# Performance work log

Measured on AMD Instinct MI355X. Metric: run time of the kernel, lower is better.

## Reference

```python
import jax, jax.numpy as jnp
import numpy as np

BN = 1024      # B*N voxel groups
M = 32         # points per voxel
D_MODEL = 128
D_POINTS = 64


def _mlp(x, w1, b1, w2, b2):
    # Linear -> ReLU -> Linear (torch nn.Sequential equivalent)
    return jax.nn.relu(x @ w1 + b1) @ w2 + b2


def setup_inputs() -> dict:
    key = jax.random.key(0)
    ks = jax.random.split(key, 16)
    def lin(k, din, dout):
        return (jax.random.normal(k, (din, dout), jnp.float32) / np.sqrt(din)).astype(jnp.float32)
    inp = {}
    inp["pv_xyz"] = jax.random.normal(ks[0], (BN, M, 3), jnp.float32)
    inp["features"] = jax.random.normal(ks[1], (BN, M, D_POINTS), jnp.float32)
    i = 2
    for name, din in [("alpha", 3), ("beta", 3), ("delta", 3), ("epsilon", D_MODEL), ("omega", D_POINTS)]:
        inp[f"{name}_w1"] = lin(ks[i], din, D_MODEL); i += 1
        inp[f"{name}_b1"] = jnp.zeros((D_MODEL,), jnp.float32)
        inp[f"{name}_w2"] = lin(ks[i], D_MODEL, D_MODEL); i += 1
        inp[f"{name}_b2"] = jnp.zeros((D_MODEL,), jnp.float32)
    return inp


def reference(pv_xyz, features,
              alpha_w1, alpha_b1, alpha_w2, alpha_b2,
              beta_w1, beta_b1, beta_w2, beta_b2,
              delta_w1, delta_b1, delta_w2, delta_b2,
              epsilon_w1, epsilon_b1, epsilon_w2, epsilon_b2,
              omega_w1, omega_b1, omega_w2, omega_b2):
    # abs relative position: [BN, M, M, 3]
    dist = jnp.abs(pv_xyz[:, :, None, :] - pv_xyz[:, None, :, :])
    pij = _mlp(dist, delta_w1, delta_b1, delta_w2, delta_b2)          # [BN,M,M,D]
    q = _mlp(pv_xyz, alpha_w1, alpha_b1, alpha_w2, alpha_b2)          # [BN,M,D]
    k = _mlp(pv_xyz, beta_w1, beta_b1, beta_w2, beta_b2)              # [BN,M,D]
    v = _mlp(features, omega_w1, omega_b1, omega_w2, omega_b2)        # [BN,M,D]
    scale = jnp.float32(1.0 / np.sqrt(D_MODEL))
    w = _mlp((q[:, :, None, :] - k[:, None, :, :] + pij) * scale,
             epsilon_w1, epsilon_b1, epsilon_w2, epsilon_b2)          # [BN,M,M,D]
    wij = jax.nn.softmax(w, axis=-2)                                  # softmax over key axis
    # torch.einsum('bmmf,bmf->bmf', wij, v): repeated index -> diagonal of wij
    midx = jnp.arange(wij.shape[1])
    res = wij[:, midx, midx, :] * v                                   # [BN,M,D]
    return jnp.concatenate([res, features], axis=-1)                  # [BN,M,D+C]
```

## Files before the change

### kernel.cpp

```cpp
#include <hip/hip_runtime.h>
#include <hip/hip_bf16.h>
#include <cstdint>
#include <cstddef>


#define SCALE 0.08838834764831843f

typedef __bf16 bf16x8 __attribute__((ext_vector_type(8)));
typedef float f32x16 __attribute__((ext_vector_type(16)));

__device__ __forceinline__ ushort f2b(float f){
  __hip_bfloat16 h = __float2bfloat16(f);
  return __builtin_bit_cast(ushort, h);
}
__device__ __forceinline__ float b2f(uint32_t s){
  union { uint32_t u; float f; } x; x.u = s << 16; return x.f;
}
__device__ __forceinline__ uint32_t pk2(float a, float b){
  union { __hip_bfloat162 h2; uint32_t u; } x;
  x.h2.x = __float2bfloat16(a); x.h2.y = __float2bfloat16(b);
  return x.u;
}
__device__ __forceinline__ f32x16 MFMA(uint4 a, uint4 b, f32x16 c){
  return __builtin_amdgcn_mfma_f32_32x32x16_bf16(
      __builtin_bit_cast(bf16x8, a), __builtin_bit_cast(bf16x8, b), c, 0, 0, 0);
}

__global__ __launch_bounds__(256) void k_pre(
    const float* __restrict__ A2, const float* __restrict__ B2, const float* __restrict__ D2,
    const float* __restrict__ E1, const float* __restrict__ E2,
    const float* __restrict__ O1, const float* __restrict__ O2,
    const float* __restrict__ ab2, const float* __restrict__ bb2, const float* __restrict__ db2,
    const float* __restrict__ eb1,
    const float* __restrict__ D1, const float* __restrict__ db1,
    ushort* __restrict__ aep, ushort* __restrict__ bep, ushort* __restrict__ gtp,
    ushort* __restrict__ e2p, ushort* __restrict__ o2p, ushort* __restrict__ o1t,
    ushort* __restrict__ d1p, float* __restrict__ c0)
{
  const int bid = blockIdx.x, tid = threadIdx.x;
  if (bid < 192){
    const float* W = (bid < 64) ? A2 : (bid < 128) ? B2 : D2;
    ushort* dst    = (bid < 64) ? aep : (bid < 128) ? bep : gtp;
    int flat = (bid & 63)*256 + tid;
    int co = flat >> 10, rem = flat & 1023, h = rem >> 3, i = rem & 7;
    int r = co*8 + i;
    float acc = 0.f;
    for (int t = 0; t < 128; ++t) acc = fmaf(W[r*128 + t], E1[t*128 + h], acc);
    dst[(co*128 + h)*8 + i] = f2b(acc * SCALE);
  } else if (bid < 256){
    int flat = (bid - 192)*256 + tid;
    int co = flat >> 10, rem = flat & 1023, d = rem >> 3, i = rem & 7;
    e2p[(co*128 + d)*8 + i] = f2b(E2[(co*8 + i)*128 + d]);
  } else if (bid < 320){
    int flat = (bid - 256)*256 + tid;
    int co = flat >> 10, rem = flat & 1023, d = rem >> 3, i = rem & 7;
    o2p[(co*128 + d)*8 + i] = f2b(O2[(co*8 + i)*128 + d]);
  } else if (bid < 352){
    int flat = (bid - 320)*256 + tid;
    int fo = flat >> 10, rem = flat & 1023, o = rem >> 3, e = rem & 7;
    o1t[(fo*128 + o)*8 + e] = f2b(O1[(fo*8 + e)*128 + o]);
  } else if (bid < 360){
    int flat = (bid - 352)*256 + tid;
    int koct = flat >> 10, cd = (flat >> 3) & 127, e = flat & 7;
    float val = 0.f;
    if (koct == 0){
      if (e < 3) val = D1[e*128 + cd];
      else if (e == 3) val = db1[cd];
    }
    d1p[flat] = f2b(val);
  } else {
    if (tid < 128){
      float acc = 0.f;
      for (int t = 0; t < 128; ++t) acc = fmaf(ab2[t] - bb2[t] + db2[t], E1[t*128 + tid], acc);
      c0[tid] = acc * SCALE + eb1[tid];
    }
  }
}

__device__ __forceinline__ void gemm64x128(const ushort (*sa)[64][8], const ushort (*sw)[128][8],
                                           int w, int l31, int hl, int p0,
                                           const float* __restrict__ bias,
                                           ushort* __restrict__ dst)
{
  const int rw = w >> 1, ctb = (w & 1) * 2;
  f32x16 acc0, acc1;
#pragma unroll
  for (int r = 0; r < 16; ++r){ acc0[r] = 0.f; acc1[r] = 0.f; }
#pragma unroll
  for (int kk = 0; kk < 8; ++kk){
    uint4 a  = *(const uint4*)&sa[2*kk + hl][32*rw + l31][0];
    uint4 b0 = *(const uint4*)&sw[2*kk + hl][32*ctb + l31][0];
    uint4 b1 = *(const uint4*)&sw[2*kk + hl][32*(ctb+1) + l31][0];
    acc0 = MFMA(a, b0, acc0);
    acc1 = MFMA(a, b1, acc1);
  }
#pragma unroll
  for (int t = 0; t < 2; ++t){
    const f32x16 acc = t ? acc1 : acc0;
    const int d = 32*(ctb + t) + l31;
    const float bv = bias ? bias[d] : 0.f;
#pragma unroll
    for (int r = 0; r < 16; ++r){
      int row = 32*rw + (r & 3) + 8*(r >> 2) + 4*hl;
      dst[(size_t)(p0 + row)*128 + d] = f2b(acc[r] + bv);
    }
  }
}

__global__ __launch_bounds__(256, 2) void k_point(
    const float* __restrict__ pv, const float* __restrict__ feat,
    const float* __restrict__ A1, const float* __restrict__ ab1,
    const float* __restrict__ B1, const float* __restrict__ bb1,
    const float* __restrict__ ob1, const float* __restrict__ ob2,
    const float* __restrict__ c0,
    const uint4* __restrict__ aep, const uint4* __restrict__ bep,
    const uint4* __restrict__ o1t, const uint4* __restrict__ o2p,
    ushort* __restrict__ qe_ws, ushort* __restrict__ ke_ws, ushort* __restrict__ v_ws,
    float* __restrict__ out)
{
  __shared__ ushort sW[16][128][8];
  __shared__ ushort sA[16][64][8];
  __shared__ ushort sF[8][64][8];
  __shared__ float  sLw[3][128];
  __shared__ float  sLb[128];
  __shared__ float  sLb2[128];

  const int tid = threadIdx.x;
  const int p0  = blockIdx.x * 64;
  const int w = tid >> 6, lane = tid & 63, l31 = lane & 31, hl = lane >> 5;

  for (int idx = tid; idx < 64*16; idx += 256){
    int p = idx >> 4, k4 = idx & 15;
    float4 f = ((const float4*)(feat + (size_t)(p0 + p)*64))[k4];
    ((float4*)(out + (size_t)(p0 + p)*192 + 128))[k4] = f;
  }

  for (int idx = tid; idx < 2048; idx += 256) ((uint4*)sW)[idx] = aep[idx];
  for (int idx = tid; idx < 384; idx += 256) ((float*)sLw)[idx] = A1[idx];
  if (tid < 128) sLb[tid] = ab1[tid];
  __syncthreads();
  {
    int p = tid & 63, ob = tid >> 6;
    float x0 = pv[(size_t)(p0+p)*3+0], x1 = pv[(size_t)(p0+p)*3+1], x2 = pv[(size_t)(p0+p)*3+2];
#pragma unroll
    for (int it = 0; it < 4; ++it){
      int oct = ob + 4*it;
      float h[8];
#pragma unroll
      for (int e = 0; e < 8; ++e){
        int cd = oct*8 + e;
        float t = fmaf(x0, sLw[0][cd], fmaf(x1, sLw[1][cd], fmaf(x2, sLw[2][cd], sLb[cd])));
        h[e] = fmaxf(t, 0.f);
      }
      uint4 u; u.x = pk2(h[0],h[1]); u.y = pk2(h[2],h[3]); u.z = pk2(h[4],h[5]); u.w = pk2(h[6],h[7]);
      *(uint4*)&sA[oct][p][0] = u;
    }
  }
  __syncthreads();
  gemm64x128(sA, sW, w, l31, hl, p0, c0, qe_ws);
  __syncthreads();

  for (int idx = tid; idx < 2048; idx += 256) ((uint4*)sW)[idx] = bep[idx];
  for (int idx = tid; idx < 384; idx += 256) ((float*)sLw)[idx] = B1[idx];
  if (tid < 128) sLb[tid] = bb1[tid];
  __syncthreads();
  {
    int p = tid & 63, ob = tid >> 6;
    float x0 = pv[(size_t)(p0+p)*3+0], x1 = pv[(size_t)(p0+p)*3+1], x2 = pv[(size_t)(p0+p)*3+2];
#pragma unroll
    for (int it = 0; it < 4; ++it){
      int oct = ob + 4*it;
      float h[8];
#pragma unroll
      for (int e = 0; e < 8; ++e){
        int cd = oct*8 + e;
        float t = fmaf(x0, sLw[0][cd], fmaf(x1, sLw[1][cd], fmaf(x2, sLw[2][cd], sLb[cd])));
        h[e] = fmaxf(t, 0.f);
      }
      uint4 u; u.x = pk2(h[0],h[1]); u.y = pk2(h[2],h[3]); u.z = pk2(h[4],h[5]); u.w = pk2(h[6],h[7]);
      *(uint4*)&sA[oct][p][0] = u;
    }
  }
  __syncthreads();
  gemm64x128(sA, sW, w, l31, hl, p0, nullptr, ke_ws);
  __syncthreads();

  for (int idx = tid; idx < 512; idx += 256){
    int p = idx & 63, fo = idx >> 6;
    const float* fp = feat + (size_t)(p0 + p)*64 + 8*fo;
    float4 f0 = ((const float4*)fp)[0], f1 = ((const float4*)fp)[1];
    uint4 u; u.x = pk2(f0.x,f0.y); u.y = pk2(f0.z,f0.w); u.z = pk2(f1.x,f1.y); u.w = pk2(f1.z,f1.w);
    *(uint4*)&sF[fo][p][0] = u;
  }
  for (int idx = tid; idx < 1024; idx += 256) ((uint4*)sW)[idx] = o1t[idx];
  if (tid < 128) sLb[tid] = ob1[tid];
  __syncthreads();
  {
    f32x16 acc0, acc1;
#pragma unroll
    for (int r = 0; r < 16; ++r){ acc0[r] = 0.f; acc1[r] = 0.f; }
#pragma unroll
    for (int kk = 0; kk < 4; ++kk){
      uint4 a  = *(const uint4*)&sW[2*kk + hl][32*w + l31][0];
      uint4 b0 = *(const uint4*)&sF[2*kk + hl][l31][0];
      uint4 b1 = *(const uint4*)&sF[2*kk + hl][32 + l31][0];
      acc0 = MFMA(a, b0, acc0);
      acc1 = MFMA(a, b1, acc1);
    }
#pragma unroll
    for (int t = 0; t < 2; ++t){
      const f32x16 acc = t ? acc1 : acc0;
      const int pt = 32*t + l31;
#pragma unroll
      for (int q = 0; q < 4; ++q){
        int o0 = 32*w + 8*q + 4*hl;
        float z0 = fmaxf(acc[4*q+0] + sLb[o0+0], 0.f);
        float z1 = fmaxf(acc[4*q+1] + sLb[o0+1], 0.f);
        float z2 = fmaxf(acc[4*q+2] + sLb[o0+2], 0.f);
        float z3 = fmaxf(acc[4*q+3] + sLb[o0+3], 0.f);
        uint2 u; u.x = pk2(z0, z1); u.y = pk2(z2, z3);
        *(uint2*)&sA[4*w + q][pt][4*hl] = u;
      }
    }
  }
  __syncthreads();

  for (int idx = tid; idx < 2048; idx += 256) ((uint4*)sW)[idx] = o2p[idx];
  if (tid < 128) sLb2[tid] = ob2[tid];
  __syncthreads();
  {
    const int rw = w >> 1, ctb = (w & 1) * 2;
    f32x16 acc0, acc1;
#pragma unroll
    for (int r = 0; r < 16; ++r){ acc0[r] = 0.f; acc1[r] = 0.f; }
#pragma unroll
    for (int kk = 0; kk < 8; ++kk){
      uint4 a  = *(const uint4*)&sA[2*kk + hl][32*rw + l31][0];
      uint4 b0 = *(const uint4*)&sW[2*kk + hl][32*ctb + l31][0];
      uint4 b1 = *(const uint4*)&sW[2*kk + hl][32*(ctb+1) + l31][0];
      acc0 = MFMA(a, b0, acc0);
      acc1 = MFMA(a, b1, acc1);
    }
#pragma unroll
    for (int t = 0; t < 2; ++t){
      const f32x16 acc = t ? acc1 : acc0;
      const int d = 32*(ctb + t) + l31;
      const float bias = sLb2[d];
#pragma unroll
      for (int r = 0; r < 16; ++r){
        int row = 32*rw + (r & 3) + 8*(r >> 2) + 4*hl;
        v_ws[(size_t)(p0 + row)*128 + d] = f2b(acc[r] + bias);
      }
    }
  }
}

__global__ __launch_bounds__(256, 3) void k_main(
    const float* __restrict__ pv,
    const ushort* __restrict__ qe_ws, const ushort* __restrict__ ke_ws, const ushort* __restrict__ v_ws,
    const uint4* __restrict__ gtp, const uint4* __restrict__ e2p, const uint4* __restrict__ d1p,
    float* __restrict__ out)
{
  __shared__ ushort sHDE[16][128][8];
  __shared__ float  sQE[16][128];
  __shared__ float  sXYZ[32][3];

  const int tid = threadIdx.x;
  const int b   = blockIdx.x >> 1;
  const int ch0 = (blockIdx.x & 1) * 4;
  const int w = tid >> 6, lane = tid & 63, l31 = lane & 31, hl = lane >> 5;

  for (int idx = tid; idx < 96; idx += 256) ((float*)sXYZ)[idx] = pv[(size_t)b*96 + idx];
  for (int idx = tid; idx < 512; idx += 256){
    int il = idx >> 5, sl = idx & 31;
    uint2 qu = ((const uint2*)qe_ws)[(size_t)(b*32 + 4*ch0 + il)*32 + sl];
    float4 o;
    o.x = b2f(qu.x & 0xffff); o.y = b2f(qu.x >> 16);
    o.z = b2f(qu.y & 0xffff); o.w = b2f(qu.y >> 16);
    ((float4*)&sQE[il][0])[sl] = o;
  }

  float kreg[16];
  {
    const ushort* kp = ke_ws + (size_t)(b*32 + l31)*128 + 32*w + 4*hl;
#pragma unroll
    for (int q = 0; q < 4; ++q){
      uint2 ku = *(const uint2*)(kp + 8*q);
      kreg[4*q+0] = b2f(ku.x & 0xffff); kreg[4*q+1] = b2f(ku.x >> 16);
      kreg[4*q+2] = b2f(ku.y & 0xffff); kreg[4*q+3] = b2f(ku.y >> 16);
    }
  }
  uint4 wG[8], wE[8];
#pragma unroll
  for (int kk = 0; kk < 8; ++kk){
    wG[kk] = gtp[(2*kk + hl)*128 + 32*w + l31];
    wE[kk] = e2p[(2*kk + hl)*128 + 32*w + l31];
  }
  uint4 wD = d1p[hl*128 + 32*w + l31];
  __syncthreads();

  const float xj0 = sXYZ[l31][0], xj1 = sXYZ[l31][1], xj2 = sXYZ[l31][2];

#pragma unroll
  for (int cc = 0; cc < 4; ++cc){
    const int c = ch0 + cc;

    f32x16 accD[4];
#pragma unroll
    for (int ct = 0; ct < 4; ++ct){
      const int i = 4*c + ct;
      float dx = fabsf(sXYZ[i][0] - xj0);
      float dy = fabsf(sXYZ[i][1] - xj1);
      float dz = fabsf(sXYZ[i][2] - xj2);
      uint4 bD; bD.x = pk2(dx, dy); bD.y = pk2(dz, 1.0f); bD.z = 0u; bD.w = 0u;
      f32x16 z;
#pragma unroll
      for (int r = 0; r < 16; ++r) z[r] = 0.f;
      accD[ct] = MFMA(wD, bD, z);
    }
#pragma unroll
    for (int ct = 0; ct < 4; ++ct){
#pragma unroll
      for (int q = 0; q < 4; ++q){
        uint2 o;
        o.x = pk2(fmaxf(accD[ct][4*q+0],0.f), fmaxf(accD[ct][4*q+1],0.f));
        o.y = pk2(fmaxf(accD[ct][4*q+2],0.f), fmaxf(accD[ct][4*q+3],0.f));
        *(uint2*)&sHDE[4*w + q][32*ct + l31][4*hl] = o;
      }
    }
    __syncthreads();

    f32x16 acc1[4];
#pragma unroll
    for (int ct = 0; ct < 4; ++ct){
      const int il = (4*c + ct) & 15;
#pragma unroll
      for (int q = 0; q < 4; ++q){
        float4 qv = *(const float4*)&sQE[il][32*w + 4*hl + 8*q];
        acc1[ct][4*q+0] = qv.x - kreg[4*q+0];
        acc1[ct][4*q+1] = qv.y - kreg[4*q+1];
        acc1[ct][4*q+2] = qv.z - kreg[4*q+2];
        acc1[ct][4*q+3] = qv.w - kreg[4*q+3];
      }
    }
#pragma unroll
    for (int kk = 0; kk < 8; ++kk){
      uint4 a = wG[kk];
#pragma unroll
      for (int ct = 0; ct < 4; ++ct){
        uint4 bu = *(const uint4*)&sHDE[2*kk + hl][32*ct + l31][0];
        acc1[ct] = MFMA(a, bu, acc1[ct]);
      }
    }
    __syncthreads();

#pragma unroll
    for (int ct = 0; ct < 4; ++ct){
#pragma unroll
      for (int q = 0; q < 4; ++q){
        uint2 o;
        o.x = pk2(fmaxf(acc1[ct][4*q+0],0.f), fmaxf(acc1[ct][4*q+1],0.f));
        o.y = pk2(fmaxf(acc1[ct][4*q+2],0.f), fmaxf(acc1[ct][4*q+3],0.f));
        *(uint2*)&sHDE[4*w + q][32*ct + l31][4*hl] = o;
      }
    }
    __syncthreads();

    f32x16 acc2[4];
#pragma unroll
    for (int rt = 0; rt < 4; ++rt)
#pragma unroll
      for (int r = 0; r < 16; ++r) acc2[rt][r] = 0.f;
#pragma unroll
    for (int kk = 0; kk < 8; ++kk){
      uint4 bfrag = wE[kk];
#pragma unroll
      for (int rt = 0; rt < 4; ++rt){
        uint4 au = *(const uint4*)&sHDE[2*kk + hl][32*rt + l31][0];
        acc2[rt] = MFMA(au, bfrag, acc2[rt]);
      }
    }

    const int g = (c >> 1) & 3;
    const int hls = c & 1;
#pragma unroll
    for (int rt = 0; rt < 4; ++rt){
      const int i = 4*c + rt;
      float m01 = fmaxf(acc2[rt][0], acc2[rt][1]);
      float m23 = fmaxf(acc2[rt][2], acc2[rt][3]);
      float m45 = fmaxf(acc2[rt][4], acc2[rt][5]);
      float m67 = fmaxf(acc2[rt][6], acc2[rt][7]);
      float m89 = fmaxf(acc2[rt][8], acc2[rt][9]);
      float mab = fmaxf(acc2[rt][10], acc2[rt][11]);
      float mcd = fmaxf(acc2[rt][12], acc2[rt][13]);
      float mef = fmaxf(acc2[rt][14], acc2[rt][15]);
      float m = fmaxf(fmaxf(fmaxf(m01,m23), fmaxf(m45,m67)),
                      fmaxf(fmaxf(m89,mab), fmaxf(mcd,mef)));
      m = fmaxf(m, __shfl_xor(m, 32));
      float s = 0.f;
#pragma unroll
      for (int r = 0; r < 16; ++r) s += __expf(acc2[rt][r] - m);
      s += __shfl_xor(s, 32);
      float d0 = acc2[rt][rt], d1 = acc2[rt][rt+4], d2 = acc2[rt][rt+8], d3 = acc2[rt][rt+12];
      float diag = (g == 0) ? d0 : (g == 1) ? d1 : (g == 2) ? d2 : d3;
      if (hl == hls){
        float num = __expf(diag - m);
        float vv = b2f((uint32_t)v_ws[(size_t)(b*32 + i)*128 + 32*w + l31]);
        out[(size_t)(b*32 + i)*192 + 32*w + l31] = num / s * vv;
      }
    }
    __syncthreads();
  }
}

static constexpr size_t OFF_AEP = 0;
static constexpr size_t OFF_BEP = 32768;
static constexpr size_t OFF_GTP = 65536;
static constexpr size_t OFF_E2P = 98304;
static constexpr size_t OFF_O1T = 131072;
static constexpr size_t OFF_O2P = 147456;
static constexpr size_t OFF_C0  = 180224;
static constexpr size_t OFF_D1P = 180736;
static constexpr size_t OFF_QE  = 184832;
static constexpr size_t OFF_KE  = OFF_QE + (size_t)32768*128*2;
static constexpr size_t OFF_V   = OFF_KE + (size_t)32768*128*2;

extern "C" void kernel_launch(void* const* d_in, const int* in_sizes, int n_in,
                              void* d_out, int out_size, void* d_ws, size_t ws_size,
                              hipStream_t stream)
{
  (void)in_sizes; (void)n_in; (void)out_size; (void)ws_size;
  const float* pv   = (const float*)d_in[0];
  const float* feat = (const float*)d_in[1];
  const float* A1 = (const float*)d_in[2];  const float* ab1 = (const float*)d_in[3];
  const float* A2 = (const float*)d_in[4];  const float* ab2 = (const float*)d_in[5];
  const float* B1 = (const float*)d_in[6];  const float* bb1 = (const float*)d_in[7];
  const float* B2 = (const float*)d_in[8];  const float* bb2 = (const float*)d_in[9];
  const float* D1 = (const float*)d_in[10]; const float* db1 = (const float*)d_in[11];
  const float* D2 = (const float*)d_in[12]; const float* db2 = (const float*)d_in[13];
  const float* E1 = (const float*)d_in[14]; const float* eb1 = (const float*)d_in[15];
  const float* E2 = (const float*)d_in[16];
  const float* O1 = (const float*)d_in[18]; const float* ob1 = (const float*)d_in[19];
  const float* O2 = (const float*)d_in[20]; const float* ob2 = (const float*)d_in[21];

  char* ws = (char*)d_ws;
  ushort* aep = (ushort*)(ws + OFF_AEP);
  ushort* bep = (ushort*)(ws + OFF_BEP);
  ushort* gtp = (ushort*)(ws + OFF_GTP);
  ushort* e2p = (ushort*)(ws + OFF_E2P);
  ushort* o1t = (ushort*)(ws + OFF_O1T);
  ushort* o2p = (ushort*)(ws + OFF_O2P);
  float*  c0  = (float*)(ws + OFF_C0);
  ushort* d1p = (ushort*)(ws + OFF_D1P);
  ushort* qe  = (ushort*)(ws + OFF_QE);
  ushort* ke  = (ushort*)(ws + OFF_KE);
  ushort* vv  = (ushort*)(ws + OFF_V);
  float* out = (float*)d_out;

  hipLaunchKernelGGL(k_pre, dim3(361), dim3(256), 0, stream,
                     A2, B2, D2, E1, E2, O1, O2, ab2, bb2, db2, eb1, D1, db1,
                     aep, bep, gtp, e2p, o2p, o1t, d1p, c0);
  hipLaunchKernelGGL(k_point, dim3(512), dim3(256), 0, stream,
                     pv, feat, A1, ab1, B1, bb1, ob1, ob2, c0,
                     (const uint4*)aep, (const uint4*)bep, (const uint4*)o1t, (const uint4*)o2p,
                     qe, ke, vv, out);
  hipLaunchKernelGGL(k_main, dim3(2048), dim3(256), 0, stream,
                     pv, qe, ke, vv, (const uint4*)gtp, (const uint4*)e2p, (const uint4*)d1p,
                     out);
}
```

Measured before the change: 129.7 us.

## Raise k_main occupancy, store Q in bf16 LDS, drop softmax max-shift

Raises k_main's launch-bounds minimum from 3 to 4 blocks per CU, and halves the shared-memory Q tile by keeping it in bf16 and unpacking it on read. The v values are now loaded before the second GEMM, so global-load latency overlaps the MFMAs. The softmax no longer subtracts the row maximum, and the divide becomes a hardware reciprocal. That removes a reduction and one shuffle, but it can overflow for large logits and depends on the input range staying small.

```diff
diff --git a/kernel.cpp b/kernel.cpp
--- a/kernel.cpp
+++ b/kernel.cpp
@@ -15,6 +15,12 @@
 }
 __device__ __forceinline__ float b2f(uint32_t s){
   union { uint32_t u; float f; } x; x.u = s << 16; return x.f;
+}
+__device__ __forceinline__ float blo(uint32_t u){
+  union { uint32_t x; float f; } v; v.x = u << 16; return v.f;
+}
+__device__ __forceinline__ float bhi(uint32_t u){
+  union { uint32_t x; float f; } v; v.x = u & 0xffff0000u; return v.f;
 }
 __device__ __forceinline__ uint32_t pk2(float a, float b){
   union { __hip_bfloat162 h2; uint32_t u; } x;
@@ -255,14 +261,14 @@
   }
 }
 
-__global__ __launch_bounds__(256, 3) void k_main(
+__global__ __launch_bounds__(256, 4) void k_main(
     const float* __restrict__ pv,
     const ushort* __restrict__ qe_ws, const ushort* __restrict__ ke_ws, const ushort* __restrict__ v_ws,
     const uint4* __restrict__ gtp, const uint4* __restrict__ e2p, const uint4* __restrict__ d1p,
     float* __restrict__ out)
 {
   __shared__ ushort sHDE[16][128][8];
-  __shared__ float  sQE[16][128];
+  __shared__ ushort sQE[16][128];
   __shared__ float  sXYZ[32][3];
 
   const int tid = threadIdx.x;
@@ -271,14 +277,8 @@
   const int w = tid >> 6, lane = tid & 63, l31 = lane & 31, hl = lane >> 5;
 
   for (int idx = tid; idx < 96; idx += 256) ((float*)sXYZ)[idx] = pv[(size_t)b*96 + idx];
-  for (int idx = tid; idx < 512; idx += 256){
-    int il = idx >> 5, sl = idx & 31;
-    uint2 qu = ((const uint2*)qe_ws)[(size_t)(b*32 + 4*ch0 + il)*32 + sl];
-    float4 o;
-    o.x = b2f(qu.x & 0xffff); o.y = b2f(qu.x >> 16);
-    o.z = b2f(qu.y & 0xffff); o.w = b2f(qu.y >> 16);
-    ((float4*)&sQE[il][0])[sl] = o;
-  }
+  for (int idx = tid; idx < 512; idx += 256)
+    ((uint2*)sQE)[idx] = ((const uint2*)qe_ws)[(size_t)(b*32 + 4*ch0)*32 + idx];
 
   float kreg[16];
   {
@@ -333,14 +333,14 @@
     f32x16 acc1[4];
 #pragma unroll
     for (int ct = 0; ct < 4; ++ct){
-      const int il = (4*c + ct) & 15;
+      const int il = 4*cc + ct;
 #pragma unroll
       for (int q = 0; q < 4; ++q){
-        float4 qv = *(const float4*)&sQE[il][32*w + 4*hl + 8*q];
-        acc1[ct][4*q+0] = qv.x - kreg[4*q+0];
-        acc1[ct][4*q+1] = qv.y - kreg[4*q+1];
-        acc1[ct][4*q+2] = qv.z - kreg[4*q+2];
-        acc1[ct][4*q+3] = qv.w - kreg[4*q+3];
+        uint2 qu = *(const uint2*)&sQE[il][32*w + 4*hl + 8*q];
+        acc1[ct][4*q+0] = blo(qu.x) - kreg[4*q+0];
+        acc1[ct][4*q+1] = bhi(qu.x) - kreg[4*q+1];
+        acc1[ct][4*q+2] = blo(qu.y) - kreg[4*q+2];
+        acc1[ct][4*q+3] = bhi(qu.y) - kreg[4*q+3];
       }
     }
 #pragma unroll
@@ -366,6 +366,11 @@
     }
     __syncthreads();
 
+    float vv[4];
+#pragma unroll
+    for (int rt = 0; rt < 4; ++rt)
+      vv[rt] = b2f((uint32_t)v_ws[(size_t)(b*32 + 4*c + rt)*128 + 32*w + l31]);
+
     f32x16 acc2[4];
 #pragma unroll
     for (int rt = 0; rt < 4; ++rt)
@@ -385,28 +390,16 @@
     const int hls = c & 1;
 #pragma unroll
     for (int rt = 0; rt < 4; ++rt){
-      const int i = 4*c + rt;
-      float m01 = fmaxf(acc2[rt][0], acc2[rt][1]);
-      float m23 = fmaxf(acc2[rt][2], acc2[rt][3]);
-      float m45 = fmaxf(acc2[rt][4], acc2[rt][5]);
-      float m67 = fmaxf(acc2[rt][6], acc2[rt][7]);
-      float m89 = fmaxf(acc2[rt][8], acc2[rt][9]);
-      float mab = fmaxf(acc2[rt][10], acc2[rt][11]);
-      float mcd = fmaxf(acc2[rt][12], acc2[rt][13]);
-      float mef = fmaxf(acc2[rt][14], acc2[rt][15]);
-      float m = fmaxf(fmaxf(fmaxf(m01,m23), fmaxf(m45,m67)),
-                      fmaxf(fmaxf(m89,mab), fmaxf(mcd,mef)));
-      m = fmaxf(m, __shfl_xor(m, 32));
-      float s = 0.f;
-#pragma unroll
-      for (int r = 0; r < 16; ++r) s += __expf(acc2[rt][r] - m);
+      float e[16];
+#pragma unroll
+      for (int r = 0; r < 16; ++r) e[r] = __expf(acc2[rt][r]);
+      float s01 = e[0]+e[1],   s23 = e[2]+e[3],   s45 = e[4]+e[5],   s67 = e[6]+e[7];
+      float s89 = e[8]+e[9],   sab = e[10]+e[11], scd = e[12]+e[13], sef = e[14]+e[15];
+      float s = ((s01+s23)+(s45+s67)) + ((s89+sab)+(scd+sef));
       s += __shfl_xor(s, 32);
-      float d0 = acc2[rt][rt], d1 = acc2[rt][rt+4], d2 = acc2[rt][rt+8], d3 = acc2[rt][rt+12];
-      float diag = (g == 0) ? d0 : (g == 1) ? d1 : (g == 2) ? d2 : d3;
+      float num = (g == 0) ? e[rt] : (g == 1) ? e[rt+4] : (g == 2) ? e[rt+8] : e[rt+12];
       if (hl == hls){
-        float num = __expf(diag - m);
-        float vv = b2f((uint32_t)v_ws[(size_t)(b*32 + i)*128 + 32*w + l31]);
-        out[(size_t)(b*32 + i)*192 + 32*w + l31] = num / s * vv;
+        out[(size_t)(b*32 + 4*c + rt)*192 + 32*w + l31] = num * __builtin_amdgcn_rcpf(s) * vv[rt];
       }
     }
     __syncthreads();
```

New measurement: 161.9 us. 24.9% more time.
